# Kernel optimization log

Hardware: AMD Instinct MI355X
Metric: run time of the kernel (lower is better)

The kernel has to match this reference:

```python
import jax, jax.numpy as jnp
import numpy as np

EPS = 1e-5

def _bn(x, g, b, m, v):
    inv = g / jnp.sqrt(v + EPS)
    return x * inv[None, :, None, None] + (b - m * inv)[None, :, None, None]

def _box_conv(x, y_min, y_max, x_min, x_max):
    # Learnable box filter via integral image + bilinear-interpolated corners.
    # x: (N, C, H, W); box params: (C, B). Output: (N, C*B, H, W), area-normalized.
    N, C, H, W = x.shape
    B = y_min.shape[1]
    # padded integral image (N, C, H+1, W+1)
    I = jnp.pad(jnp.cumsum(jnp.cumsum(x, axis=2), axis=3), ((0, 0), (0, 0), (1, 0), (1, 0)))
    iy = jnp.arange(H, dtype=x.dtype)
    ix = jnp.arange(W, dtype=x.dtype)

    def one_box(Ic, ymn, ymx, xmn, xmx):
        # Ic: (N, H+1, W+1); scalar box extents
        y1 = jnp.clip(iy + ymn, 0.0, H)
        y2 = jnp.clip(iy + ymx + 1.0, 0.0, H)
        x1 = jnp.clip(ix + xmn, 0.0, W)
        x2 = jnp.clip(ix + xmx + 1.0, 0.0, W)

        def interp_y(c):  # (H,) -> (N, H, W+1)
            i0 = jnp.clip(jnp.floor(c), 0.0, H - 1).astype(jnp.int32)
            t = (c - i0)[None, :, None]
            return Ic[:, i0, :] * (1.0 - t) + Ic[:, i0 + 1, :] * t

        Gy1, Gy2 = interp_y(y1), interp_y(y2)

        def interp_x(G, c):  # (N, H, W+1), (W,) -> (N, H, W)
            i0 = jnp.clip(jnp.floor(c), 0.0, W - 1).astype(jnp.int32)
            t = (c - i0)[None, None, :]
            return G[:, :, i0] * (1.0 - t) + G[:, :, i0 + 1] * t

        S = interp_x(Gy2, x2) - interp_x(Gy2, x1) - interp_x(Gy1, x2) + interp_x(Gy1, x1)
        area = (ymx - ymn + 1.0) * (xmx - xmn + 1.0)
        return S / area  # (N, H, W)

    f_b = jax.vmap(one_box, in_axes=(None, 0, 0, 0, 0))   # over boxes
    f_cb = jax.vmap(f_b, in_axes=(1, 0, 0, 0, 0))          # over channels
    out = f_cb(I, y_min, y_max, x_min, x_max)              # (C, B, N, H, W)
    return jnp.transpose(out, (2, 0, 1, 3, 4)).reshape(N, C * B, H, W)


def setup_inputs() -> dict:
    key = jax.random.key(0)
    ks = jax.random.split(key, 20)
    N, Cin, H, W = 32, 256, 56, 56
    Cmid, B = 16, 4
    Cbox = Cmid * B
    Cout = 256
    f32 = jnp.float32
    x = jax.random.normal(ks[0], (N, Cin, H, W), f32)
    w1 = jax.random.normal(ks[1], (Cmid, Cin), f32) * 0.05
    g1 = jax.random.uniform(ks[2], (Cmid,), f32, 0.5, 1.5)
    b1 = jax.random.normal(ks[3], (Cmid,), f32) * 0.1
    m1 = jax.random.normal(ks[4], (Cmid,), f32) * 0.1
    v1 = jax.random.uniform(ks[5], (Cmid,), f32, 0.5, 1.5)
    y_min = -jax.random.uniform(ks[6], (Cmid, B), f32) * 10.0
    y_max = jax.random.uniform(ks[7], (Cmid, B), f32) * 10.0
    x_min = -jax.random.uniform(ks[8], (Cmid, B), f32) * 10.0
    x_max = jax.random.uniform(ks[9], (Cmid, B), f32) * 10.0
    g2 = jax.random.uniform(ks[10], (Cbox,), f32, 0.5, 1.5)
    b2 = jax.random.normal(ks[11], (Cbox,), f32) * 0.1
    m2 = jax.random.normal(ks[12], (Cbox,), f32) * 0.1
    v2 = jax.random.uniform(ks[13], (Cbox,), f32, 0.5, 1.5)
    w3 = jax.random.normal(ks[14], (Cout, Cbox), f32) * 0.05
    g3 = jax.random.uniform(ks[15], (Cout,), f32, 0.5, 1.5)
    b3 = jax.random.normal(ks[16], (Cout,), f32) * 0.1
    m3 = jax.random.normal(ks[17], (Cout,), f32) * 0.1
    v3 = jax.random.uniform(ks[18], (Cout,), f32, 0.5, 1.5)
    return {"x": x, "w1": w1, "g1": g1, "b1": b1, "m1": m1, "v1": v1,
            "y_min": y_min, "y_max": y_max, "x_min": x_min, "x_max": x_max,
            "g2": g2, "b2": b2, "m2": m2, "v2": v2,
            "w3": w3, "g3": g3, "b3": b3, "m3": m3, "v3": v3}


def reference(x, w1, g1, b1, m1, v1, y_min, y_max, x_min, x_max,
              g2, b2, m2, v2, w3, g3, b3, m3, v3):
    out = jnp.einsum('nchw,oc->nohw', x, w1)            # 1x1 conv
    out = jax.nn.relu(_bn(out, g1, b1, m1, v1))
    out = _box_conv(out, y_min, y_max, x_min, x_max)    # (N, Cmid*B, H, W)
    out = jax.nn.relu(_bn(out, g2, b2, m2, v2))
    out = jnp.einsum('nchw,oc->nohw', out, w3)          # 1x1 conv
    out = _bn(out, g3, b3, m3, v3)
    return jax.nn.relu(out + x)
```

## Files before the change

kernel.cpp:

```cpp
#include <hip/hip_runtime.h>
#include <hip/hip_bf16.h>
#include <math.h>

#define EPSB 1e-5f

constexpr int NN = 32, CIN = 256, HH = 56, WW = 56, HW = HH * WW;
constexpr int CMID = 16, NB = 4, CBOX = 64, COUT = 256;

typedef __attribute__((ext_vector_type(8))) short short8;
typedef __attribute__((ext_vector_type(4))) float f32x4;

constexpr size_t WS_INV3  = 0;
constexpr size_t WS_B3F   = WS_INV3 + COUT;
constexpr size_t WS_W3B   = WS_B3F + COUT;
constexpr size_t WS_OUT1B = WS_W3B + (size_t)CBOX * COUT / 2;
constexpr size_t WS_OUT2B = WS_OUT1B + (size_t)NN * CMID * HW / 2;

__global__ __launch_bounds__(256) void k1(const float* __restrict__ x,
                                          const float* __restrict__ w1,
                                          const float* __restrict__ g1,
                                          const float* __restrict__ b1,
                                          const float* __restrict__ m1,
                                          const float* __restrict__ v1,
                                          const float* __restrict__ w3,
                                          const float* __restrict__ g3,
                                          const float* __restrict__ b3,
                                          const float* __restrict__ m3,
                                          const float* __restrict__ v3,
                                          float* __restrict__ ws,
                                          __hip_bfloat16* __restrict__ out1b) {
  __shared__ __hip_bfloat16 Xb[64][264];
  __shared__ __hip_bfloat16 Wb[16][264];
  int bid = blockIdx.x;
  int n = bid / 49, hwb = (bid % 49) * 64;
  int tid = threadIdx.x;
  int l = tid & 63, w = tid >> 6;

  if (bid == 0) {
    __hip_bfloat16* w3b = (__hip_bfloat16*)(ws + WS_W3B);
    const float* wp = w3 + tid * 64;
#pragma unroll
    for (int j = 0; j < 64; j += 8) {
      f32x4 a = *reinterpret_cast<const f32x4*>(wp + j);
      f32x4 b = *reinterpret_cast<const f32x4*>(wp + j + 4);
      union { short8 s; __hip_bfloat16 h[8]; } u;
#pragma unroll
      for (int q = 0; q < 4; ++q) { u.h[q] = __float2bfloat16(a[q]); u.h[q + 4] = __float2bfloat16(b[q]); }
      *reinterpret_cast<short8*>(w3b + tid * 64 + j) = u.s;
    }
    float iv = g3[tid] / sqrtf(v3[tid] + EPSB);
    ws[WS_INV3 + tid] = iv;
    ws[WS_B3F + tid] = b3[tid] - m3[tid] * iv;
  }

  {
    int c = tid >> 4, kb = (tid & 15) * 16;
    float inv = g1[c] / sqrtf(v1[c] + EPSB);
    const float* wp = w1 + c * CIN + kb;
    f32x4 a[4];
#pragma unroll
    for (int q = 0; q < 4; ++q) a[q] = *reinterpret_cast<const f32x4*>(wp + q * 4);
    union { short8 s[2]; __hip_bfloat16 h[16]; } u;
#pragma unroll
    for (int j = 0; j < 16; ++j) u.h[j] = __float2bfloat16(a[j >> 2][j & 3] * inv);
    *reinterpret_cast<short8*>(&Wb[c][kb]) = u.s[0];
    *reinterpret_cast<short8*>(&Wb[c][kb + 8]) = u.s[1];
  }

  {
    const float* xb = x + (size_t)n * CIN * HW + hwb;
    int px0 = (tid & 15) * 4, ci0 = (tid >> 4) * 16;
#pragma unroll
    for (int hh = 0; hh < 2; ++hh) {
      int cb = ci0 + hh * 8;
      f32x4 v[8];
#pragma unroll
      for (int cj = 0; cj < 8; ++cj)
        v[cj] = *reinterpret_cast<const f32x4*>(xb + (size_t)(cb + cj) * HW + px0);
#pragma unroll
      for (int pj = 0; pj < 4; ++pj) {
        union { short8 s; __hip_bfloat16 h[8]; } u;
#pragma unroll
        for (int cj = 0; cj < 8; ++cj) u.h[cj] = __float2bfloat16(v[cj][pj]);
        *reinterpret_cast<short8*>(&Xb[px0 + pj][cb]) = u.s;
      }
    }
  }
  __syncthreads();

  int pix = 16 * w + (l & 15);
  f32x4 acc = (f32x4)(0.f);
#pragma unroll
  for (int kk = 0; kk < 8; ++kk) {
    int k0 = kk * 32 + (l >> 4) * 8;
    short8 xfr = *reinterpret_cast<const short8*>(&Xb[pix][k0]);
    short8 wfr = *reinterpret_cast<const short8*>(&Wb[l & 15][k0]);
    acc = __builtin_amdgcn_mfma_f32_16x16x32_bf16(xfr, wfr, acc, 0, 0, 0);
  }

  {
    int c = l & 15;
    int px = 16 * w + (l >> 4) * 4;
    float inv = g1[c] / sqrtf(v1[c] + EPSB);
    float bb = b1[c] - m1[c] * inv;
    union { unsigned long long v; __hip_bfloat16 h[4]; } o;
#pragma unroll
    for (int j = 0; j < 4; ++j) o.h[j] = __float2bfloat16(fmaxf(acc[j] + bb, 0.f));
    *reinterpret_cast<unsigned long long*>(out1b + ((size_t)n * CMID + c) * HW + hwb + px) = o.v;
  }
}

__device__ __forceinline__ float bilin(const float* __restrict__ sI, float y, float x) {
  int iy = min((int)y, 55);
  int ix = min((int)x, 55);
  float ty = y - (float)iy;
  float tx = x - (float)ix;
  const float* r = sI + iy * 57 + ix;
  float a = r[0], b = r[1], cc = r[57], d = r[58];
  float g1v = a * (1.f - ty) + cc * ty;
  float g2v = b * (1.f - ty) + d * ty;
  return g1v * (1.f - tx) + g2v * tx;
}

__global__ __launch_bounds__(512) void k2(
    const __hip_bfloat16* __restrict__ out1b,
    const float* __restrict__ y_min, const float* __restrict__ y_max,
    const float* __restrict__ x_min, const float* __restrict__ x_max,
    const float* __restrict__ g2, const float* __restrict__ b2,
    const float* __restrict__ m2, const float* __restrict__ v2,
    __hip_bfloat16* __restrict__ out2b) {
  __shared__ float sI[57 * 57];
  int bid = blockIdx.x;
  int n = bid >> 4, c = bid & 15;
  int tid = threadIdx.x;
  int lane = tid & 63, w = tid >> 6;

  if (tid < 57) { sI[tid] = 0.f; sI[tid * 57] = 0.f; }
  const __hip_bfloat16* src = out1b + ((size_t)n * CMID + c) * HW;
  if (tid < HW / 8) {
    int p = tid * 8;
    int h = p / 56, wq = p - h * 56;
    short8 d = ((const short8*)src)[tid];
    const __hip_bfloat16* dp = (const __hip_bfloat16*)&d;
    float* dst = &sI[(h + 1) * 57 + wq + 1];
#pragma unroll
    for (int j = 0; j < 8; ++j) dst[j] = __bfloat162float(dp[j]);
  }
  __syncthreads();

  for (int r = w; r < 56; r += 8) {
    float* row = &sI[(r + 1) * 57 + 1];
    float vv = (lane < 56) ? row[lane] : 0.f;
#pragma unroll
    for (int d = 1; d < 64; d <<= 1) {
      float o = __shfl_up(vv, d, 64);
      if (lane >= d) vv += o;
    }
    if (lane < 56) row[lane] = vv;
  }
  __syncthreads();
  for (int cc = w; cc < 56; cc += 8) {
    float* col = &sI[57 + cc + 1];
    float vv = (lane < 56) ? col[lane * 57] : 0.f;
#pragma unroll
    for (int d = 1; d < 64; d <<= 1) {
      float o = __shfl_up(vv, d, 64);
      if (lane >= d) vv += o;
    }
    if (lane < 56) col[lane * 57] = vv;
  }
  __syncthreads();

  float pymn[NB], pymx[NB], pxmn[NB], pxmx[NB], pinv[NB], pbi[NB], prar[NB];
#pragma unroll
  for (int b = 0; b < NB; ++b) {
    int cb = c * NB + b;
    pymn[b] = y_min[cb]; pymx[b] = y_max[cb];
    pxmn[b] = x_min[cb]; pxmx[b] = x_max[cb];
    float inv = g2[cb] / sqrtf(v2[cb] + EPSB);
    pinv[b] = inv;
    pbi[b] = b2[cb] - m2[cb] * inv;
    prar[b] = 1.f / ((pymx[b] - pymn[b] + 1.f) * (pxmx[b] - pxmn[b] + 1.f));
  }
  __hip_bfloat16* dst0 = out2b + ((size_t)n * CBOX + c * NB) * HW;

  for (int p = tid; p < HW; p += 512) {
    int h = p / 56, wq = p - h * 56;
    float fh = (float)h, fw = (float)wq;
#pragma unroll
    for (int b = 0; b < NB; ++b) {
      float y1 = fminf(fmaxf(fh + pymn[b], 0.f), 56.f);
      float y2 = fminf(fmaxf(fh + pymx[b] + 1.f, 0.f), 56.f);
      float x1 = fminf(fmaxf(fw + pxmn[b], 0.f), 56.f);
      float x2 = fminf(fmaxf(fw + pxmx[b] + 1.f, 0.f), 56.f);
      float S = bilin(sI, y2, x2) - bilin(sI, y2, x1) - bilin(sI, y1, x2) + bilin(sI, y1, x1);
      float val = S * prar[b] * pinv[b] + pbi[b];
      dst0[(size_t)b * HW + p] = __float2bfloat16(fmaxf(val, 0.f));
    }
  }
}

__global__ __launch_bounds__(512) void k3(
    const __hip_bfloat16* __restrict__ out2b,
    const __hip_bfloat16* __restrict__ w3b,
    const float* __restrict__ inv3, const float* __restrict__ b3f,
    const float* __restrict__ x, float* __restrict__ out) {
  __shared__ __hip_bfloat16 T[64][72];
  int bid = blockIdx.x;
  int n = bid / 49, hwb = (bid % 49) * 64;
  int tid = threadIdx.x;
  int l = tid & 63, w = tid >> 6;

  {
    const __hip_bfloat16* srcp = out2b + ((size_t)n * CBOX + l) * HW + hwb + w * 8;
    short8 v = *reinterpret_cast<const short8*>(srcp);
    const __hip_bfloat16* vp = (const __hip_bfloat16*)&v;
#pragma unroll
    for (int i = 0; i < 8; ++i) T[w * 8 + i][l] = vp[i];
  }

  short8 wfrag[2][2];
#pragma unroll
  for (int ot = 0; ot < 2; ++ot)
#pragma unroll
    for (int kh = 0; kh < 2; ++kh) {
      int o = w * 32 + ot * 16 + (l & 15);
      int k0 = kh * 32 + (l >> 4) * 8;
      wfrag[ot][kh] = *reinterpret_cast<const short8*>(w3b + o * CBOX + k0);
    }

  __syncthreads();

  short8 tfrag[4][2];
#pragma unroll
  for (int pt = 0; pt < 4; ++pt)
#pragma unroll
    for (int kh = 0; kh < 2; ++kh) {
      int pix = pt * 16 + (l & 15);
      int k0 = kh * 32 + (l >> 4) * 8;
      tfrag[pt][kh] = *reinterpret_cast<const short8*>(&T[pix][k0]);
    }

  f32x4 acc[4][2];
#pragma unroll
  for (int pt = 0; pt < 4; ++pt)
#pragma unroll
    for (int ot = 0; ot < 2; ++ot) acc[pt][ot] = (f32x4)(0.f);

#pragma unroll
  for (int pt = 0; pt < 4; ++pt)
#pragma unroll
    for (int ot = 0; ot < 2; ++ot) {
      acc[pt][ot] = __builtin_amdgcn_mfma_f32_16x16x32_bf16(
          tfrag[pt][0], wfrag[ot][0], acc[pt][ot], 0, 0, 0);
      acc[pt][ot] = __builtin_amdgcn_mfma_f32_16x16x32_bf16(
          tfrag[pt][1], wfrag[ot][1], acc[pt][ot], 0, 0, 0);
    }

  size_t nbase = (size_t)n * COUT * HW + hwb;
#pragma unroll
  for (int ot = 0; ot < 2; ++ot) {
    int o = w * 32 + ot * 16 + (l & 15);
    float iv = inv3[o];
    float bb = b3f[o];
    size_t rowbase = nbase + (size_t)o * HW;
#pragma unroll
    for (int pt = 0; pt < 4; ++pt) {
      int px0 = pt * 16 + (l >> 4) * 4;
      f32x4 xv = *reinterpret_cast<const f32x4*>(x + rowbase + px0);
      f32x4 r;
#pragma unroll
      for (int j = 0; j < 4; ++j)
        r[j] = fmaxf(acc[pt][ot][j] * iv + bb + xv[j], 0.f);
      *reinterpret_cast<f32x4*>(out + rowbase + px0) = r;
    }
  }
}

extern "C" void kernel_launch(void* const* d_in, const int* in_sizes, int n_in,
                              void* d_out, int out_size, void* d_ws, size_t ws_size,
                              hipStream_t stream) {
  const float* x   = (const float*)d_in[0];
  const float* w1  = (const float*)d_in[1];
  const float* g1  = (const float*)d_in[2];
  const float* b1  = (const float*)d_in[3];
  const float* m1  = (const float*)d_in[4];
  const float* v1  = (const float*)d_in[5];
  const float* ymn = (const float*)d_in[6];
  const float* ymx = (const float*)d_in[7];
  const float* xmn = (const float*)d_in[8];
  const float* xmx = (const float*)d_in[9];
  const float* g2  = (const float*)d_in[10];
  const float* b2  = (const float*)d_in[11];
  const float* m2  = (const float*)d_in[12];
  const float* v2  = (const float*)d_in[13];
  const float* w3  = (const float*)d_in[14];
  const float* g3  = (const float*)d_in[15];
  const float* b3  = (const float*)d_in[16];
  const float* m3  = (const float*)d_in[17];
  const float* v3  = (const float*)d_in[18];

  float* ws  = (float*)d_ws;
  float* out = (float*)d_out;
  __hip_bfloat16* out1b = (__hip_bfloat16*)(ws + WS_OUT1B);
  __hip_bfloat16* out2b = (__hip_bfloat16*)(ws + WS_OUT2B);
  __hip_bfloat16* w3b   = (__hip_bfloat16*)(ws + WS_W3B);

  k1<<<NN * 49, 256, 0, stream>>>(x, w1, g1, b1, m1, v1,
                                  w3, g3, b3, m3, v3, ws, out1b);
  k2<<<NN * CMID, 512, 0, stream>>>(out1b, ymn, ymx, xmn, xmx,
                                    g2, b2, m2, v2, out2b);
  k3<<<NN * 49, 512, 0, stream>>>(out2b, w3b, ws + WS_INV3, ws + WS_B3F, x, out);
}
```

Baseline: 82.45 us.

## Load conv1 operands directly into MFMA fragments and streamline box-filter interpolation

The first kernel no longer stages x and w1 through shared memory. Each lane now loads its own weight fragments and gathers eight channel values per pixel straight from global memory into registers before each MFMA, which removes the LDS writes, the reads and the barrier. In exchange the x loads become scalar strided loads, coalesced across 16 lanes, instead of wide vector loads. The box kernel inlines the bilinear lookups in lerp form and replaces the per-iteration divide by 56 with incremental row and column updates.

```diff
diff --git a/kernel.cpp b/kernel.cpp
--- a/kernel.cpp
+++ b/kernel.cpp
@@ -29,8 +29,6 @@
                                           const float* __restrict__ v3,
                                           float* __restrict__ ws,
                                           __hip_bfloat16* __restrict__ out1b) {
-  __shared__ __hip_bfloat16 Xb[64][264];
-  __shared__ __hip_bfloat16 Wb[16][264];
   int bid = blockIdx.x;
   int n = bid / 49, hwb = (bid % 49) * 64;
   int tid = threadIdx.x;
@@ -53,73 +51,47 @@
     ws[WS_B3F + tid] = b3[tid] - m3[tid] * iv;
   }
 
+  int c = l & 15;
+  int kq = (l >> 4) * 8;
+
+  float inv1 = g1[c] / sqrtf(v1[c] + EPSB);
+  short8 bfrag[8];
+#pragma unroll
+  for (int kk = 0; kk < 8; ++kk) {
+    const float* wp = w1 + c * CIN + kk * 32 + kq;
+    f32x4 a = *reinterpret_cast<const f32x4*>(wp);
+    f32x4 b = *reinterpret_cast<const f32x4*>(wp + 4);
+    union { short8 s; __hip_bfloat16 h[8]; } u;
+#pragma unroll
+    for (int q = 0; q < 4; ++q) {
+      u.h[q]     = __float2bfloat16(a[q] * inv1);
+      u.h[q + 4] = __float2bfloat16(b[q] * inv1);
+    }
+    bfrag[kk] = u.s;
+  }
+
+  const float* xb = x + (size_t)n * CIN * HW + hwb + 16 * w + (l & 15);
+  f32x4 acc = (f32x4)(0.f);
+#pragma unroll
+  for (int kk = 0; kk < 8; ++kk) {
+    const float* xp = xb + (size_t)(kk * 32 + kq) * HW;
+    float v[8];
+#pragma unroll
+    for (int j = 0; j < 8; ++j) v[j] = xp[(size_t)j * HW];
+    union { short8 s; __hip_bfloat16 h[8]; } u;
+#pragma unroll
+    for (int j = 0; j < 8; ++j) u.h[j] = __float2bfloat16(v[j]);
+    acc = __builtin_amdgcn_mfma_f32_16x16x32_bf16(u.s, bfrag[kk], acc, 0, 0, 0);
+  }
+
   {
-    int c = tid >> 4, kb = (tid & 15) * 16;
-    float inv = g1[c] / sqrtf(v1[c] + EPSB);
-    const float* wp = w1 + c * CIN + kb;
-    f32x4 a[4];
-#pragma unroll
-    for (int q = 0; q < 4; ++q) a[q] = *reinterpret_cast<const f32x4*>(wp + q * 4);
-    union { short8 s[2]; __hip_bfloat16 h[16]; } u;
-#pragma unroll
-    for (int j = 0; j < 16; ++j) u.h[j] = __float2bfloat16(a[j >> 2][j & 3] * inv);
-    *reinterpret_cast<short8*>(&Wb[c][kb]) = u.s[0];
-    *reinterpret_cast<short8*>(&Wb[c][kb + 8]) = u.s[1];
-  }
-
-  {
-    const float* xb = x + (size_t)n * CIN * HW + hwb;
-    int px0 = (tid & 15) * 4, ci0 = (tid >> 4) * 16;
-#pragma unroll
-    for (int hh = 0; hh < 2; ++hh) {
-      int cb = ci0 + hh * 8;
-      f32x4 v[8];
-#pragma unroll
-      for (int cj = 0; cj < 8; ++cj)
-        v[cj] = *reinterpret_cast<const f32x4*>(xb + (size_t)(cb + cj) * HW + px0);
-#pragma unroll
-      for (int pj = 0; pj < 4; ++pj) {
-        union { short8 s; __hip_bfloat16 h[8]; } u;
-#pragma unroll
-        for (int cj = 0; cj < 8; ++cj) u.h[cj] = __float2bfloat16(v[cj][pj]);
-        *reinterpret_cast<short8*>(&Xb[px0 + pj][cb]) = u.s;
-      }
-    }
-  }
-  __syncthreads();
-
-  int pix = 16 * w + (l & 15);
-  f32x4 acc = (f32x4)(0.f);
-#pragma unroll
-  for (int kk = 0; kk < 8; ++kk) {
-    int k0 = kk * 32 + (l >> 4) * 8;
-    short8 xfr = *reinterpret_cast<const short8*>(&Xb[pix][k0]);
-    short8 wfr = *reinterpret_cast<const short8*>(&Wb[l & 15][k0]);
-    acc = __builtin_amdgcn_mfma_f32_16x16x32_bf16(xfr, wfr, acc, 0, 0, 0);
-  }
-
-  {
-    int c = l & 15;
+    float bb = b1[c] - m1[c] * inv1;
     int px = 16 * w + (l >> 4) * 4;
-    float inv = g1[c] / sqrtf(v1[c] + EPSB);
-    float bb = b1[c] - m1[c] * inv;
     union { unsigned long long v; __hip_bfloat16 h[4]; } o;
 #pragma unroll
     for (int j = 0; j < 4; ++j) o.h[j] = __float2bfloat16(fmaxf(acc[j] + bb, 0.f));
     *reinterpret_cast<unsigned long long*>(out1b + ((size_t)n * CMID + c) * HW + hwb + px) = o.v;
   }
-}
-
-__device__ __forceinline__ float bilin(const float* __restrict__ sI, float y, float x) {
-  int iy = min((int)y, 55);
-  int ix = min((int)x, 55);
-  float ty = y - (float)iy;
-  float tx = x - (float)ix;
-  const float* r = sI + iy * 57 + ix;
-  float a = r[0], b = r[1], cc = r[57], d = r[58];
-  float g1v = a * (1.f - ty) + cc * ty;
-  float g2v = b * (1.f - ty) + d * ty;
-  return g1v * (1.f - tx) + g2v * tx;
 }
 
 __global__ __launch_bounds__(512) void k2(
@@ -184,19 +156,41 @@
   }
   __hip_bfloat16* dst0 = out2b + ((size_t)n * CBOX + c * NB) * HW;
 
-  for (int p = tid; p < HW; p += 512) {
-    int h = p / 56, wq = p - h * 56;
+  int p = tid;
+  int h = p / 56, wq = p - h * 56;
+  for (; p < HW; ) {
     float fh = (float)h, fw = (float)wq;
 #pragma unroll
     for (int b = 0; b < NB; ++b) {
-      float y1 = fminf(fmaxf(fh + pymn[b], 0.f), 56.f);
-      float y2 = fminf(fmaxf(fh + pymx[b] + 1.f, 0.f), 56.f);
-      float x1 = fminf(fmaxf(fw + pxmn[b], 0.f), 56.f);
-      float x2 = fminf(fmaxf(fw + pxmx[b] + 1.f, 0.f), 56.f);
-      float S = bilin(sI, y2, x2) - bilin(sI, y2, x1) - bilin(sI, y1, x2) + bilin(sI, y1, x1);
+      float y1c = fminf(fmaxf(fh + pymn[b], 0.f), 56.f);
+      float y2c = fminf(fmaxf(fh + pymx[b] + 1.f, 0.f), 56.f);
+      float x1c = fminf(fmaxf(fw + pxmn[b], 0.f), 56.f);
+      float x2c = fminf(fmaxf(fw + pxmx[b] + 1.f, 0.f), 56.f);
+      int iy1 = min((int)y1c, 55), iy2 = min((int)y2c, 55);
+      int ix1 = min((int)x1c, 55), ix2 = min((int)x2c, 55);
+      float ty1 = y1c - (float)iy1, ty2 = y2c - (float)iy2;
+      float sx1 = x1c - (float)ix1, sx2 = x2c - (float)ix2;
+      const float* r2a = sI + iy2 * 57;
+      const float* r1a = sI + iy1 * 57;
+      float t22 = r2a[ix2] + (r2a[ix2 + 1] - r2a[ix2]) * sx2;
+      float u22 = r2a[ix2 + 57] + (r2a[ix2 + 58] - r2a[ix2 + 57]) * sx2;
+      float c22 = t22 + (u22 - t22) * ty2;
+      float t21 = r2a[ix1] + (r2a[ix1 + 1] - r2a[ix1]) * sx1;
+      float u21 = r2a[ix1 + 57] + (r2a[ix1 + 58] - r2a[ix1 + 57]) * sx1;
+      float c21 = t21 + (u21 - t21) * ty2;
+      float t12 = r1a[ix2] + (r1a[ix2 + 1] - r1a[ix2]) * sx2;
+      float u12 = r1a[ix2 + 57] + (r1a[ix2 + 58] - r1a[ix2 + 57]) * sx2;
+      float c12 = t12 + (u12 - t12) * ty1;
+      float t11 = r1a[ix1] + (r1a[ix1 + 1] - r1a[ix1]) * sx1;
+      float u11 = r1a[ix1 + 57] + (r1a[ix1 + 58] - r1a[ix1 + 57]) * sx1;
+      float c11 = t11 + (u11 - t11) * ty1;
+
+      float S = (c22 - c21) - (c12 - c11);
       float val = S * prar[b] * pinv[b] + pbi[b];
       dst0[(size_t)b * HW + p] = __float2bfloat16(fmaxf(val, 0.f));
     }
+    p += 512; h += 9; wq += 8;
+    if (wq >= 56) { wq -= 56; h += 1; }
   }
 }
 
```

Measured after the change: 87.38 us. 1.06x slower.
